# Kernel optimization log

Hardware: AMD Instinct MI355X
Metric: run time of the kernel (lower is better)

## Reference

```python
import jax, jax.numpy as jnp
import numpy as np

B, N, M = 2, 2048, 2048
Q_DIM = 1024
HEADS = 8
DIM_HEAD = 64
INNER = HEADS * DIM_HEAD  # 512


def setup_inputs() -> dict:
    key = jax.random.key(0)
    ks = jax.random.split(key, 7)
    s_in = 1.0 / np.sqrt(Q_DIM)
    s_out = 1.0 / np.sqrt(INNER)
    return {
        "x": jax.random.normal(ks[0], (B, N, Q_DIM), dtype=jnp.float32),
        "context": jax.random.normal(ks[1], (B, M, Q_DIM), dtype=jnp.float32),
        "Wq": jax.random.normal(ks[2], (Q_DIM, INNER), dtype=jnp.float32) * s_in,
        "Wk": jax.random.normal(ks[3], (Q_DIM, INNER), dtype=jnp.float32) * s_in,
        "Wv": jax.random.normal(ks[4], (Q_DIM, INNER), dtype=jnp.float32) * s_in,
        "Wo": jax.random.normal(ks[5], (INNER, Q_DIM), dtype=jnp.float32) * s_out,
        "bo": jax.random.normal(ks[6], (Q_DIM,), dtype=jnp.float32) * 0.01,
    }


def reference(x, context, Wq, Wk, Wv, Wo, bo):
    scale = DIM_HEAD ** (-0.5)
    # projections, split heads: [b, n, inner] -> [b, h, n, d]
    def split_heads(t):
        b, n, _ = t.shape
        return t.reshape(b, n, HEADS, DIM_HEAD).transpose(0, 2, 1, 3)
    q = split_heads(x @ Wq)
    k = split_heads(context @ Wk)
    v = split_heads(context @ Wv)
    sim = jnp.einsum('bhid,bhjd->bhij', q, k) * scale  # [b,h,n,m] full score matrix
    attn = jax.nn.softmax(sim, axis=-1)
    out = jnp.einsum('bhij,bhjd->bhid', attn, v)       # [b,h,n,d]
    out = out.transpose(0, 2, 1, 3).reshape(x.shape[0], x.shape[1], INNER)
    return out @ Wo + bo
```

## Files before the change

kernel.cpp:

```cpp
#include <hip/hip_runtime.h>

typedef __attribute__((ext_vector_type(8))) short short8;
typedef __attribute__((ext_vector_type(4))) short bf16x4;
typedef __attribute__((ext_vector_type(4))) float floatx4;
typedef __attribute__((ext_vector_type(4))) float f32x4;

__device__ __forceinline__ short f2bf(float f) {
    union { float f; unsigned u; } v;
    v.f = f;
    unsigned r = v.u + 0x7fffu + ((v.u >> 16) & 1u);
    return (short)(r >> 16);
}
__device__ __forceinline__ short8 cvt8(f32x4 a, f32x4 b) {
    short8 r;
    r[0] = f2bf(a[0]); r[1] = f2bf(a[1]); r[2] = f2bf(a[2]); r[3] = f2bf(a[3]);
    r[4] = f2bf(b[0]); r[5] = f2bf(b[1]); r[6] = f2bf(b[2]); r[7] = f2bf(b[3]);
    return r;
}
__device__ __forceinline__ bf16x4 pack4(float a, float b, float c, float d) {
    union { float f; unsigned u; } x;
    unsigned ua, ub, uc, ud;
    x.f = a; ua = (x.u + 0x8000u) >> 16;
    x.f = b; ub = (x.u + 0x8000u) >> 16;
    x.f = c; uc = (x.u + 0x8000u) >> 16;
    x.f = d; ud = (x.u + 0x8000u) >> 16;
    union { bf16x4 s; unsigned u2[2]; } r;
    r.u2[0] = ua | (ub << 16);
    r.u2[1] = uc | (ud << 16);
    return r.s;
}

#define MFMA_BF16(a, b, c) __builtin_amdgcn_mfma_f32_16x16x32_bf16((a), (b), (c), 0, 0, 0)

__device__ __forceinline__ floatx4 mfma16(bf16x4 a, bf16x4 b, floatx4 c) {
#if __has_builtin(__builtin_amdgcn_mfma_f32_16x16x16bf16_1k)
    return __builtin_amdgcn_mfma_f32_16x16x16bf16_1k(a, b, c, 0, 0, 0);
#else
    floatx4 d;
    asm volatile("v_mfma_f32_16x16x16_bf16 %0, %1, %2, %3"
                 : "=&v"(d) : "v"(a), "v"(b), "v"(c));
    return d;
#endif
}

__device__ __forceinline__ float fast_exp2(float x) {
#if __has_builtin(__builtin_amdgcn_exp2f)
    return __builtin_amdgcn_exp2f(x);
#else
    return exp2f(x);
#endif
}

#define QSCALE_LOG2E 0.18033688011112042f

#define TPAD 40

__global__ __launch_bounds__(256) void transpose_all(const float* __restrict__ Wq,
                                                     const float* __restrict__ Wk,
                                                     const float* __restrict__ Wv,
                                                     const float* __restrict__ Wo,
                                                     short* __restrict__ WqT,
                                                     short* __restrict__ WkT,
                                                     short* __restrict__ WvT,
                                                     short* __restrict__ WoT) {
    const int z = blockIdx.z;
    const float* src = (z == 0) ? Wq : (z == 1) ? Wk : (z == 2) ? Wv : Wo;
    short* dst = (z == 0) ? WqT : (z == 1) ? WkT : (z == 2) ? WvT : WoT;
    const int R = (z < 3) ? 1024 : 512;
    const int C = (z < 3) ? 512 : 1024;
    const int c0 = blockIdx.x * 32;
    const int r0 = blockIdx.y * 32;
    if (c0 >= C || r0 >= R) return;
    __shared__ float tile[32][33];
    const int tx = threadIdx.x;
    const int ty = threadIdx.y;
#pragma unroll
    for (int i = 0; i < 32; i += 8)
        tile[ty + i][tx] = src[(r0 + ty + i) * C + c0 + tx];
    __syncthreads();
#pragma unroll
    for (int i = 0; i < 32; i += 8)
        dst[(c0 + ty + i) * R + r0 + tx] = f2bf(tile[tx][ty + i]);
}

__global__ __launch_bounds__(256, 3) void gemm_qkv(const float* __restrict__ x,
                                                   const float* __restrict__ ctx,
                                                   const short* __restrict__ WqT,
                                                   const short* __restrict__ WkT,
                                                   const short* __restrict__ WvT,
                                                   short* __restrict__ Qw,
                                                   short* __restrict__ Kw,
                                                   short* __restrict__ Vtw) {
    const int z = blockIdx.z;
    const float* A  = (z == 0) ? x : ctx;
    const short* WT = (z == 0) ? WqT : (z == 1) ? WkT : WvT;
    const int tid = threadIdx.x;
    const int w = tid >> 6;
    const int lane = tid & 63;
    const int quad = lane >> 4, ln = lane & 15;
    const int wr = w >> 1, wc = w & 1;
    const int row0 = blockIdx.x * 64;
    const int col0 = blockIdx.y * 128;

    __shared__ __align__(16) short Alds[2][64][TPAD];
    __shared__ __align__(16) short Blds[2][128][TPAD];

    const int srow = tid >> 2;
    const int scol = (tid & 3) * 8;
    const float* aG = A + (size_t)(row0 + srow) * 1024 + scol;
    const short* bG0 = WT + (size_t)(col0 + srow) * 1024 + scol;
    const short* bG1 = WT + (size_t)(col0 + srow + 64) * 1024 + scol;

    floatx4 acc[2][4] = {};
    f32x4 aR[2][2];
    short8 bR[2][2];

    auto loadStep = [&](int it, int set) {
        const int kk = it * 32;
        aR[set][0] = *(const f32x4*)(aG + kk);
        aR[set][1] = *(const f32x4*)(aG + kk + 4);
        bR[set][0] = *(const short8*)(bG0 + kk);
        bR[set][1] = *(const short8*)(bG1 + kk);
    };
    auto writeStep = [&](int buf, int set) {
        *(short8*)(&Alds[buf][srow][scol]) = cvt8(aR[set][0], aR[set][1]);
        *(short8*)(&Blds[buf][srow][scol]) = bR[set][0];
        *(short8*)(&Blds[buf][srow + 64][scol]) = bR[set][1];
    };

    loadStep(0, 0);
    writeStep(0, 0);
    loadStep(1, 1);
    __syncthreads();

    const int nsteps = 1024 / 32;
    for (int it = 0; it < nsteps; ++it) {
        const int buf = it & 1;
        if (it + 2 < nsteps) loadStep(it + 2, it & 1);
        if (it + 1 < nsteps) writeStep(buf ^ 1, (it + 1) & 1);
        short8 af[2], bf4[4];
#pragma unroll
        for (int i = 0; i < 2; ++i)
            af[i] = *(const short8*)(&Alds[buf][wr * 32 + i * 16 + ln][quad * 8]);
#pragma unroll
        for (int t = 0; t < 4; ++t)
            bf4[t] = *(const short8*)(&Blds[buf][wc * 64 + t * 16 + ln][quad * 8]);
#pragma unroll
        for (int i = 0; i < 2; ++i)
#pragma unroll
            for (int t = 0; t < 4; ++t)
                acc[i][t] = MFMA_BF16(af[i], bf4[t], acc[i][t]);
        __syncthreads();
    }

    const float oscale = (z == 0) ? QSCALE_LOG2E : 1.0f;
    short* dst = (z == 0) ? Qw : (z == 1) ? Kw : Vtw;
#pragma unroll
    for (int i = 0; i < 2; ++i)
#pragma unroll
        for (int t = 0; t < 4; ++t)
#pragma unroll
            for (int r = 0; r < 4; ++r) {
                const int R = row0 + wr * 32 + i * 16 + quad * 4 + r;
                const int C = col0 + wc * 64 + t * 16 + ln;
                const int b = R >> 11, n = R & 2047;
                const int h = C >> 6, d = C & 63;
                const short val = f2bf(acc[i][t][r] * oscale);
                if (z < 2)
                    dst[((b * 8 + h) * 2048 + n) * 64 + d] = val;
                else
                    dst[((b * 8 + h) * 64 + d) * 2048 + n] = val;
            }
}

__global__ __launch_bounds__(256, 2) void attn_kernel(const short* __restrict__ Q,
                                                      const short* __restrict__ K,
                                                      const short* __restrict__ Vt,
                                                      short* __restrict__ Aw) {
    const int tid = threadIdx.x;
    const int w = tid >> 6;
    const int lane = tid & 63;
    const int quad = lane >> 4;
    const int ln = lane & 15;
    const int q0 = blockIdx.x * 64;
    const int bh = blockIdx.y;

    __shared__ __align__(16) short klds[2][64][72];
    __shared__ __align__(16) short vlds[2][64][72];

    const short* Qbh = Q + bh * 2048 * 64;
    const short* Kbh = K + bh * 2048 * 64;
    const short* Vbh = Vt + bh * 64 * 2048;

    short8 qf[2];
    {
        const int qrow = q0 + w * 16 + ln;
        qf[0] = *(const short8*)(Qbh + qrow * 64 + quad * 8);
        qf[1] = *(const short8*)(Qbh + qrow * 64 + 32 + quad * 8);
    }

    floatx4 ot[4] = {};
    float lp = 0.f;

    const int sr = tid >> 3;
    const int sc = (tid & 7) * 8;

    auto computeTile = [&](int b) {
        short8 kf[8];
#pragma unroll
        for (int t = 0; t < 4; ++t)
#pragma unroll
            for (int ks = 0; ks < 2; ++ks)
                kf[t * 2 + ks] = *(const short8*)(&klds[b][t * 16 + ln][ks * 32 + quad * 8]);
        bf16x4 vf[16];
#pragma unroll
        for (int dt = 0; dt < 4; ++dt)
#pragma unroll
            for (int t = 0; t < 4; ++t)
                vf[dt * 4 + t] = *(const bf16x4*)(&vlds[b][dt * 16 + ln][t * 16 + quad * 4]);

        floatx4 s[4] = {};
#pragma unroll
        for (int ks = 0; ks < 2; ++ks)
#pragma unroll
            for (int t = 0; t < 4; ++t)
                s[t] = MFMA_BF16(kf[t * 2 + ks], qf[ks], s[t]);

        bf16x4 pf[4];
#pragma unroll
        for (int t = 0; t < 4; ++t) {
            float p0 = fast_exp2(s[t][0]);
            float p1 = fast_exp2(s[t][1]);
            float p2 = fast_exp2(s[t][2]);
            float p3 = fast_exp2(s[t][3]);
            lp += (p0 + p1) + (p2 + p3);
            pf[t] = pack4(p0, p1, p2, p3);
        }
#pragma unroll
        for (int t = 0; t < 4; ++t)
#pragma unroll
            for (int dt = 0; dt < 4; ++dt)
                ot[dt] = mfma16(vf[dt * 4 + t], pf[t], ot[dt]);
    };

    const int nt = 2048 / 64;

    {
        short8 k0 = *(const short8*)(Kbh + tid * 8);
        short8 k1 = *(const short8*)(Kbh + (tid + 256) * 8);
        short8 v0 = *(const short8*)(Vbh + sr * 2048 + sc);
        short8 v1 = *(const short8*)(Vbh + (sr + 32) * 2048 + sc);
        *(short8*)(&klds[0][sr][sc]) = k0;
        *(short8*)(&klds[0][sr + 32][sc]) = k1;
        *(short8*)(&vlds[0][sr][sc]) = v0;
        *(short8*)(&vlds[0][sr + 32][sc]) = v1;
    }
    __syncthreads();

    for (int it = 0; it < nt; ++it) {
        short8 k0, k1, v0, v1;
        const bool more = (it + 1 < nt);
        if (more) {
            const int jn = (it + 1) * 64;
            k0 = *(const short8*)(Kbh + jn * 64 + tid * 8);
            k1 = *(const short8*)(Kbh + jn * 64 + (tid + 256) * 8);
            v0 = *(const short8*)(Vbh + sr * 2048 + jn + sc);
            v1 = *(const short8*)(Vbh + (sr + 32) * 2048 + jn + sc);
        }
        computeTile(it & 1);
        if (more) {
            const int nb = (it + 1) & 1;
            *(short8*)(&klds[nb][sr][sc]) = k0;
            *(short8*)(&klds[nb][sr + 32][sc]) = k1;
            *(short8*)(&vlds[nb][sr][sc]) = v0;
            *(short8*)(&vlds[nb][sr + 32][sc]) = v1;
        }
        __syncthreads();
    }

    lp += __shfl_xor(lp, 16);
    lp += __shfl_xor(lp, 32);
    const float invL = 1.0f / lp;

    const int n = q0 + w * 16 + ln;
    const int b = bh >> 3, h = bh & 7;
    short* abase = Aw + ((size_t)(b * 2048 + n) * 512) + h * 64 + quad * 4;
#pragma unroll
    for (int dt = 0; dt < 4; ++dt)
        *(bf16x4*)(abase + dt * 16) =
            pack4(ot[dt][0] * invL, ot[dt][1] * invL, ot[dt][2] * invL, ot[dt][3] * invL);
}

__global__ __launch_bounds__(256, 3) void gemm_final(const short* __restrict__ A,
                                                     const short* __restrict__ WoT,
                                                     const float* __restrict__ bias,
                                                     float* __restrict__ out) {
    const int tid = threadIdx.x;
    const int w = tid >> 6;
    const int lane = tid & 63;
    const int quad = lane >> 4, ln = lane & 15;
    const int wr = w >> 1, wc = w & 1;
    const int row0 = blockIdx.x * 64;
    const int col0 = blockIdx.y * 128;

    __shared__ __align__(16) short Alds[2][64][TPAD];
    __shared__ __align__(16) short Blds[2][128][TPAD];

    const int srow = tid >> 2;
    const int scol = (tid & 3) * 8;
    const short* aG = A + (size_t)(row0 + srow) * 512 + scol;
    const short* bG0 = WoT + (size_t)(col0 + srow) * 512 + scol;
    const short* bG1 = WoT + (size_t)(col0 + srow + 64) * 512 + scol;

    floatx4 acc[2][4] = {};
    short8 aR[2];
    short8 bR[2][2];

    auto loadStep = [&](int it, int set) {
        const int kk = it * 32;
        aR[set]    = *(const short8*)(aG + kk);
        bR[set][0] = *(const short8*)(bG0 + kk);
        bR[set][1] = *(const short8*)(bG1 + kk);
    };
    auto writeStep = [&](int buf, int set) {
        *(short8*)(&Alds[buf][srow][scol]) = aR[set];
        *(short8*)(&Blds[buf][srow][scol]) = bR[set][0];
        *(short8*)(&Blds[buf][srow + 64][scol]) = bR[set][1];
    };

    loadStep(0, 0);
    writeStep(0, 0);
    loadStep(1, 1);
    __syncthreads();

    const int nsteps = 512 / 32;
    for (int it = 0; it < nsteps; ++it) {
        const int buf = it & 1;
        if (it + 2 < nsteps) loadStep(it + 2, it & 1);
        if (it + 1 < nsteps) writeStep(buf ^ 1, (it + 1) & 1);
        short8 af[2], bf4[4];
#pragma unroll
        for (int i = 0; i < 2; ++i)
            af[i] = *(const short8*)(&Alds[buf][wr * 32 + i * 16 + ln][quad * 8]);
#pragma unroll
        for (int t = 0; t < 4; ++t)
            bf4[t] = *(const short8*)(&Blds[buf][wc * 64 + t * 16 + ln][quad * 8]);
#pragma unroll
        for (int i = 0; i < 2; ++i)
#pragma unroll
            for (int t = 0; t < 4; ++t)
                acc[i][t] = MFMA_BF16(af[i], bf4[t], acc[i][t]);
        __syncthreads();
    }

#pragma unroll
    for (int i = 0; i < 2; ++i)
#pragma unroll
        for (int t = 0; t < 4; ++t)
#pragma unroll
            for (int r = 0; r < 4; ++r) {
                const int R = row0 + wr * 32 + i * 16 + quad * 4 + r;
                const int C = col0 + wc * 64 + t * 16 + ln;
                out[(size_t)R * 1024 + C] = acc[i][t][r] + bias[C];
            }
}

extern "C" void kernel_launch(void* const* d_in, const int* in_sizes, int n_in,
                              void* d_out, int out_size, void* d_ws, size_t ws_size,
                              hipStream_t stream) {
    const float* x   = (const float*)d_in[0];
    const float* ctx = (const float*)d_in[1];
    const float* Wq  = (const float*)d_in[2];
    const float* Wk  = (const float*)d_in[3];
    const float* Wv  = (const float*)d_in[4];
    const float* Wo  = (const float*)d_in[5];
    const float* bo  = (const float*)d_in[6];
    float* out = (float*)d_out;

    char* ws = (char*)d_ws;
    size_t off = 0;
    auto alloc = [&](size_t bytes) { char* p = ws + off; off += (bytes + 255) & ~(size_t)255; return p; };

    short* WqT  = (short*)alloc(512 * 1024 * 2);
    short* WkT  = (short*)alloc(512 * 1024 * 2);
    short* WvT  = (short*)alloc(512 * 1024 * 2);
    short* WoT  = (short*)alloc(1024 * 512 * 2);
    short* Qw   = (short*)alloc((size_t)16 * 2048 * 64 * 2);
    short* Kw   = (short*)alloc((size_t)16 * 2048 * 64 * 2);
    short* Vtw  = (short*)alloc((size_t)16 * 2048 * 64 * 2);
    short* Aw   = (short*)alloc((size_t)4096 * 512 * 2);

    transpose_all<<<dim3(32, 32, 4), dim3(32, 8), 0, stream>>>(Wq, Wk, Wv, Wo, WqT, WkT, WvT, WoT);

    gemm_qkv<<<dim3(64, 4, 3), 256, 0, stream>>>(x, ctx, WqT, WkT, WvT, Qw, Kw, Vtw);

    attn_kernel<<<dim3(32, 16), 256, 0, stream>>>(Qw, Kw, Vtw, Aw);

    gemm_final<<<dim3(64, 8), 256, 0, stream>>>(Aw, WoT, bo, out);
}
```

Before: 168.9 us.

## Pre-pack weights into MFMA fragment layout and load B directly to registers

```diff
diff --git a/kernel.cpp b/kernel.cpp
--- a/kernel.cpp
+++ b/kernel.cpp
@@ -53,47 +53,40 @@
 
 #define QSCALE_LOG2E 0.18033688011112042f
 
-#define TPAD 40
-
-__global__ __launch_bounds__(256) void transpose_all(const float* __restrict__ Wq,
-                                                     const float* __restrict__ Wk,
-                                                     const float* __restrict__ Wv,
-                                                     const float* __restrict__ Wo,
-                                                     short* __restrict__ WqT,
-                                                     short* __restrict__ WkT,
-                                                     short* __restrict__ WvT,
-                                                     short* __restrict__ WoT) {
-    const int z = blockIdx.z;
+__global__ __launch_bounds__(256) void wfrag_all(const float* __restrict__ Wq,
+                                                 const float* __restrict__ Wk,
+                                                 const float* __restrict__ Wv,
+                                                 const float* __restrict__ Wo,
+                                                 short* __restrict__ WqF,
+                                                 short* __restrict__ WkF,
+                                                 short* __restrict__ WvF,
+                                                 short* __restrict__ WoF) {
+    const int z = blockIdx.y;
     const float* src = (z == 0) ? Wq : (z == 1) ? Wk : (z == 2) ? Wv : Wo;
-    short* dst = (z == 0) ? WqT : (z == 1) ? WkT : (z == 2) ? WvT : WoT;
-    const int R = (z < 3) ? 1024 : 512;
-    const int C = (z < 3) ? 512 : 1024;
-    const int c0 = blockIdx.x * 32;
-    const int r0 = blockIdx.y * 32;
-    if (c0 >= C || r0 >= R) return;
-    __shared__ float tile[32][33];
-    const int tx = threadIdx.x;
-    const int ty = threadIdx.y;
-#pragma unroll
-    for (int i = 0; i < 32; i += 8)
-        tile[ty + i][tx] = src[(r0 + ty + i) * C + c0 + tx];
-    __syncthreads();
-#pragma unroll
-    for (int i = 0; i < 32; i += 8)
-        dst[(c0 + ty + i) * R + r0 + tx] = f2bf(tile[tx][ty + i]);
+    short* dst = (z == 0) ? WqF : (z == 1) ? WkF : (z == 2) ? WvF : WoF;
+    const int nbits = (z < 3) ? 9 : 10;
+    const int N = 1 << nbits;
+    const int t = blockIdx.x * 256 + threadIdx.x;
+    const int kb = t >> nbits;
+    const int n = t & (N - 1);
+    const float* s = src + (size_t)(kb * 8) * N + n;
+    short8 v;
+#pragma unroll
+    for (int j = 0; j < 8; ++j) v[j] = f2bf(s[(size_t)j * N]);
+    *(short8*)(dst + (size_t)t * 8) = v;
 }
 
 __global__ __launch_bounds__(256, 3) void gemm_qkv(const float* __restrict__ x,
                                                    const float* __restrict__ ctx,
-                                                   const short* __restrict__ WqT,
-                                                   const short* __restrict__ WkT,
-                                                   const short* __restrict__ WvT,
+                                                   const short* __restrict__ WqF,
+                                                   const short* __restrict__ WkF,
+                                                   const short* __restrict__ WvF,
                                                    short* __restrict__ Qw,
                                                    short* __restrict__ Kw,
                                                    short* __restrict__ Vtw) {
     const int z = blockIdx.z;
     const float* A  = (z == 0) ? x : ctx;
-    const short* WT = (z == 0) ? WqT : (z == 1) ? WkT : WvT;
+    const short* WF = (z == 0) ? WqF : (z == 1) ? WkF : WvF;
     const int tid = threadIdx.x;
     const int w = tid >> 6;
     const int lane = tid & 63;
@@ -102,54 +95,57 @@
     const int row0 = blockIdx.x * 64;
     const int col0 = blockIdx.y * 128;
 
-    __shared__ __align__(16) short Alds[2][64][TPAD];
-    __shared__ __align__(16) short Blds[2][128][TPAD];
+    __shared__ __align__(16) short Alds[2][2048];
 
     const int srow = tid >> 2;
-    const int scol = (tid & 3) * 8;
-    const float* aG = A + (size_t)(row0 + srow) * 1024 + scol;
-    const short* bG0 = WT + (size_t)(col0 + srow) * 1024 + scol;
-    const short* bG1 = WT + (size_t)(col0 + srow + 64) * 1024 + scol;
+    const int sseg = tid & 3;
+    const float* aG = A + (size_t)(row0 + srow) * 1024 + sseg * 8;
+
+    const short* bG[4];
+#pragma unroll
+    for (int t = 0; t < 4; ++t)
+        bG[t] = WF + ((size_t)quad * 512 + col0 + wc * 64 + t * 16 + ln) * 8;
 
     floatx4 acc[2][4] = {};
     f32x4 aR[2][2];
-    short8 bR[2][2];
-
-    auto loadStep = [&](int it, int set) {
-        const int kk = it * 32;
-        aR[set][0] = *(const f32x4*)(aG + kk);
-        aR[set][1] = *(const f32x4*)(aG + kk + 4);
-        bR[set][0] = *(const short8*)(bG0 + kk);
-        bR[set][1] = *(const short8*)(bG1 + kk);
-    };
-    auto writeStep = [&](int buf, int set) {
-        *(short8*)(&Alds[buf][srow][scol]) = cvt8(aR[set][0], aR[set][1]);
-        *(short8*)(&Blds[buf][srow][scol]) = bR[set][0];
-        *(short8*)(&Blds[buf][srow + 64][scol]) = bR[set][1];
-    };
-
-    loadStep(0, 0);
-    writeStep(0, 0);
-    loadStep(1, 1);
+    short8 bR[2][4];
+
+    auto loadA = [&](int it, int set) {
+        aR[set][0] = *(const f32x4*)(aG + it * 32);
+        aR[set][1] = *(const f32x4*)(aG + it * 32 + 4);
+    };
+    auto writeA = [&](int buf, int set) {
+        *(short8*)(&Alds[buf][(sseg * 64 + srow) * 8]) = cvt8(aR[set][0], aR[set][1]);
+    };
+    auto loadB = [&](int it, int set) {
+#pragma unroll
+        for (int t = 0; t < 4; ++t)
+            bR[set][t] = *(const short8*)(bG[t] + (size_t)it * 16384);
+    };
+
+    loadA(0, 0);
+    writeA(0, 0);
+    loadA(1, 1);
+    loadB(0, 0);
     __syncthreads();
 
     const int nsteps = 1024 / 32;
     for (int it = 0; it < nsteps; ++it) {
         const int buf = it & 1;
-        if (it + 2 < nsteps) loadStep(it + 2, it & 1);
-        if (it + 1 < nsteps) writeStep(buf ^ 1, (it + 1) & 1);
-        short8 af[2], bf4[4];
+        if (it + 2 < nsteps) loadA(it + 2, it & 1);
+        if (it + 1 < nsteps) {
+            loadB(it + 1, (it + 1) & 1);
+            writeA(buf ^ 1, (it + 1) & 1);
+        }
+        short8 af[2];
 #pragma unroll
         for (int i = 0; i < 2; ++i)
-            af[i] = *(const short8*)(&Alds[buf][wr * 32 + i * 16 + ln][quad * 8]);
-#pragma unroll
-        for (int t = 0; t < 4; ++t)
-            bf4[t] = *(const short8*)(&Blds[buf][wc * 64 + t * 16 + ln][quad * 8]);
+            af[i] = *(const short8*)(&Alds[buf][quad * 512 + (wr * 32 + i * 16 + ln) * 8]);
 #pragma unroll
         for (int i = 0; i < 2; ++i)
 #pragma unroll
             for (int t = 0; t < 4; ++t)
-                acc[i][t] = MFMA_BF16(af[i], bf4[t], acc[i][t]);
+                acc[i][t] = MFMA_BF16(af[i], bR[it & 1][t], acc[i][t]);
         __syncthreads();
     }
 
@@ -291,8 +287,8 @@
             pack4(ot[dt][0] * invL, ot[dt][1] * invL, ot[dt][2] * invL, ot[dt][3] * invL);
 }
 
-__global__ __launch_bounds__(256, 3) void gemm_final(const short* __restrict__ A,
-                                                     const short* __restrict__ WoT,
+__global__ __launch_bounds__(256, 2) void gemm_final(const short* __restrict__ A,
+                                                     const short* __restrict__ WoF,
                                                      const float* __restrict__ bias,
                                                      float* __restrict__ out) {
     const int tid = threadIdx.x;
@@ -303,53 +299,54 @@
     const int row0 = blockIdx.x * 64;
     const int col0 = blockIdx.y * 128;
 
-    __shared__ __align__(16) short Alds[2][64][TPAD];
-    __shared__ __align__(16) short Blds[2][128][TPAD];
+    __shared__ __align__(16) short Alds[2][2048];
 
     const int srow = tid >> 2;
-    const int scol = (tid & 3) * 8;
-    const short* aG = A + (size_t)(row0 + srow) * 512 + scol;
-    const short* bG0 = WoT + (size_t)(col0 + srow) * 512 + scol;
-    const short* bG1 = WoT + (size_t)(col0 + srow + 64) * 512 + scol;
+    const int sseg = tid & 3;
+    const short* aG = A + (size_t)(row0 + srow) * 512 + sseg * 8;
+
+    const short* bG[4];
+#pragma unroll
+    for (int t = 0; t < 4; ++t)
+        bG[t] = WoF + ((size_t)quad * 1024 + col0 + wc * 64 + t * 16 + ln) * 8;
 
     floatx4 acc[2][4] = {};
     short8 aR[2];
-    short8 bR[2][2];
-
-    auto loadStep = [&](int it, int set) {
-        const int kk = it * 32;
-        aR[set]    = *(const short8*)(aG + kk);
-        bR[set][0] = *(const short8*)(bG0 + kk);
-        bR[set][1] = *(const short8*)(bG1 + kk);
-    };
-    auto writeStep = [&](int buf, int set) {
-        *(short8*)(&Alds[buf][srow][scol]) = aR[set];
-        *(short8*)(&Blds[buf][srow][scol]) = bR[set][0];
-        *(short8*)(&Blds[buf][srow + 64][scol]) = bR[set][1];
-    };
-
-    loadStep(0, 0);
-    writeStep(0, 0);
-    loadStep(1, 1);
+    short8 bR[2][4];
+
+    auto loadA = [&](int it, int set) { aR[set] = *(const short8*)(aG + it * 32); };
+    auto writeA = [&](int buf, int set) {
+        *(short8*)(&Alds[buf][(sseg * 64 + srow) * 8]) = aR[set];
+    };
+    auto loadB = [&](int it, int set) {
+#pragma unroll
+        for (int t = 0; t < 4; ++t)
+            bR[set][t] = *(const short8*)(bG[t] + (size_t)it * 32768);
+    };
+
+    loadA(0, 0);
+    writeA(0, 0);
+    loadA(1, 1);
+    loadB(0, 0);
     __syncthreads();
 
     const int nsteps = 512 / 32;
     for (int it = 0; it < nsteps; ++it) {
         const int buf = it & 1;
-        if (it + 2 < nsteps) loadStep(it + 2, it & 1);
-        if (it + 1 < nsteps) writeStep(buf ^ 1, (it + 1) & 1);
-        short8 af[2], bf4[4];
+        if (it + 2 < nsteps) loadA(it + 2, it & 1);
+        if (it + 1 < nsteps) {
+            loadB(it + 1, (it + 1) & 1);
+            writeA(buf ^ 1, (it + 1) & 1);
+        }
+        short8 af[2];
 #pragma unroll
         for (int i = 0; i < 2; ++i)
-            af[i] = *(const short8*)(&Alds[buf][wr * 32 + i * 16 + ln][quad * 8]);
-#pragma unroll
-        for (int t = 0; t < 4; ++t)
-            bf4[t] = *(const short8*)(&Blds[buf][wc * 64 + t * 16 + ln][quad * 8]);
+            af[i] = *(const short8*)(&Alds[buf][quad * 512 + (wr * 32 + i * 16 + ln) * 8]);
 #pragma unroll
         for (int i = 0; i < 2; ++i)
 #pragma unroll
             for (int t = 0; t < 4; ++t)
-                acc[i][t] = MFMA_BF16(af[i], bf4[t], acc[i][t]);
+                acc[i][t] = MFMA_BF16(af[i], bR[it & 1][t], acc[i][t]);
         __syncthreads();
     }
 
@@ -381,20 +378,20 @@
     size_t off = 0;
     auto alloc = [&](size_t bytes) { char* p = ws + off; off += (bytes + 255) & ~(size_t)255; return p; };
 
-    short* WqT  = (short*)alloc(512 * 1024 * 2);
-    short* WkT  = (short*)alloc(512 * 1024 * 2);
-    short* WvT  = (short*)alloc(512 * 1024 * 2);
-    short* WoT  = (short*)alloc(1024 * 512 * 2);
+    short* WqF  = (short*)alloc(512 * 1024 * 2);
+    short* WkF  = (short*)alloc(512 * 1024 * 2);
+    short* WvF  = (short*)alloc(512 * 1024 * 2);
+    short* WoF  = (short*)alloc(1024 * 512 * 2);
     short* Qw   = (short*)alloc((size_t)16 * 2048 * 64 * 2);
     short* Kw   = (short*)alloc((size_t)16 * 2048 * 64 * 2);
     short* Vtw  = (short*)alloc((size_t)16 * 2048 * 64 * 2);
     short* Aw   = (short*)alloc((size_t)4096 * 512 * 2);
 
-    transpose_all<<<dim3(32, 32, 4), dim3(32, 8), 0, stream>>>(Wq, Wk, Wv, Wo, WqT, WkT, WvT, WoT);
-
-    gemm_qkv<<<dim3(64, 4, 3), 256, 0, stream>>>(x, ctx, WqT, WkT, WvT, Qw, Kw, Vtw);
+    wfrag_all<<<dim3(256, 4), 256, 0, stream>>>(Wq, Wk, Wv, Wo, WqF, WkF, WvF, WoF);
+
+    gemm_qkv<<<dim3(64, 4, 3), 256, 0, stream>>>(x, ctx, WqF, WkF, WvF, Qw, Kw, Vtw);
 
     attn_kernel<<<dim3(32, 16), 256, 0, stream>>>(Qw, Kw, Vtw, Aw);
 
-    gemm_final<<<dim3(64, 8), 256, 0, stream>>>(Aw, WoT, bo, out);
-}
+    gemm_final<<<dim3(64, 8), 256, 0, stream>>>(Aw, WoF, bo, out);
+}
```

New measurement: 167.9 us. About the same (-0.6%).
